# Kernel optimization log

Hardware: AMD Instinct MI355X
Metric: run time of the kernel (lower is better)

The kernel has to match this reference:

```python
import jax, jax.numpy as jnp
import numpy as np

# 3D PGA grade slices over the 16-component multivector (contiguous in standard basis order)
GRADE_SLICES = [(0, 1), (1, 5), (5, 11), (11, 15), (15, 16)]
GRADE_DIMS = [1, 4, 6, 4, 1]


def setup_inputs() -> dict:
    key = jax.random.key(0)
    ks = jax.random.split(key, 11)
    x = jax.random.normal(ks[0], (8, 2048, 128, 16), dtype=jnp.float32)
    inp = {"x": x}
    for g, d in enumerate(GRADE_DIMS):
        # match nn.Linear default init scale ~ U(-1/sqrt(d), 1/sqrt(d)); randn is fine for a numeric baseline
        inp[f"w{g}"] = jax.random.normal(ks[1 + 2 * g], (d, d), dtype=jnp.float32) / np.sqrt(d)
        inp[f"b{g}"] = jax.random.normal(ks[2 + 2 * g], (d,), dtype=jnp.float32) / np.sqrt(d)
    return inp


def reference(x, w0, b0, w1, b1, w2, b2, w3, b3, w4, b4):
    ws = [w0, w1, w2, w3, w4]
    bs = [b0, b1, b2, b3, b4]
    # Block-diagonal per-grade linear: gather slice, y = x_g @ W_g^T + b_g, scatter back.
    # Since grade index sets are contiguous, scatter == concatenate along last dim.
    outs = []
    for (lo, hi), w, b in zip(GRADE_SLICES, ws, bs):
        xg = x[..., lo:hi]                       # [..., d_g]
        outs.append(jnp.einsum("...i,oi->...o", xg, w) + b)
    return jnp.concatenate(outs, axis=-1)        # [..., 16]
```

## Files before the change

kernel.cpp:

```cpp
#include <hip/hip_runtime.h>


__global__ __launch_bounds__(256) void GradeWiseLinear_kernel(
    const float* __restrict__ x,
    const float* __restrict__ w0, const float* __restrict__ b0,
    const float* __restrict__ w1, const float* __restrict__ b1,
    const float* __restrict__ w2, const float* __restrict__ b2,
    const float* __restrict__ w3, const float* __restrict__ b3,
    const float* __restrict__ w4, const float* __restrict__ b4,
    float* __restrict__ out, int n4)
{
    __shared__ float s[86];
    {
        int t = threadIdx.x;
        if (t < 86) {
            float v;
            if      (t == 0)  v = w0[0];
            else if (t < 17)  v = w1[t - 1];
            else if (t < 53)  v = w2[t - 17];
            else if (t < 69)  v = w3[t - 53];
            else if (t == 69) v = w4[0];
            else if (t == 70) v = b0[0];
            else if (t < 75)  v = b1[t - 71];
            else if (t < 81)  v = b2[t - 75];
            else if (t < 85)  v = b3[t - 81];
            else              v = b4[0];
            s[t] = v;
        }
    }
    __syncthreads();

    int g = blockIdx.x * 256 + threadIdx.x;
    if (g >= n4) return;

    const int j = g & 3;
    const float4* x4 = (const float4*)x;

    float4 me = x4[g];
    float4 up = x4[g - (int)(j > 0)];
    float4 dn = x4[g + (int)(j < 3)];

    float o0, o1, o2, o3;

    if (j == 0) {
        o0 = s[70] + me.x * s[0];
        o1 = s[71] + me.y * s[1] + me.z * s[2]  + me.w * s[3]  + dn.x * s[4];
        o2 = s[72] + me.y * s[5] + me.z * s[6]  + me.w * s[7]  + dn.x * s[8];
        o3 = s[73] + me.y * s[9] + me.z * s[10] + me.w * s[11] + dn.x * s[12];
    } else if (j == 1) {
        o0 = s[74] + up.y * s[13] + up.z * s[14] + up.w * s[15] + me.x * s[16];
        o1 = s[75] + me.y * s[17] + me.z * s[18] + me.w * s[19]
                   + dn.x * s[20] + dn.y * s[21] + dn.z * s[22];
        o2 = s[76] + me.y * s[23] + me.z * s[24] + me.w * s[25]
                   + dn.x * s[26] + dn.y * s[27] + dn.z * s[28];
        o3 = s[77] + me.y * s[29] + me.z * s[30] + me.w * s[31]
                   + dn.x * s[32] + dn.y * s[33] + dn.z * s[34];
    } else if (j == 2) {
        o0 = s[78] + up.y * s[35] + up.z * s[36] + up.w * s[37]
                   + me.x * s[38] + me.y * s[39] + me.z * s[40];
        o1 = s[79] + up.y * s[41] + up.z * s[42] + up.w * s[43]
                   + me.x * s[44] + me.y * s[45] + me.z * s[46];
        o2 = s[80] + up.y * s[47] + up.z * s[48] + up.w * s[49]
                   + me.x * s[50] + me.y * s[51] + me.z * s[52];
        o3 = s[81] + me.w * s[53] + dn.x * s[54] + dn.y * s[55] + dn.z * s[56];
    } else {
        o0 = s[82] + up.w * s[57] + me.x * s[58] + me.y * s[59] + me.z * s[60];
        o1 = s[83] + up.w * s[61] + me.x * s[62] + me.y * s[63] + me.z * s[64];
        o2 = s[84] + up.w * s[65] + me.x * s[66] + me.y * s[67] + me.z * s[68];
        o3 = s[85] + me.w * s[69];
    }

    ((float4*)out)[g] = make_float4(o0, o1, o2, o3);
}

extern "C" void kernel_launch(void* const* d_in, const int* in_sizes, int n_in,
                              void* d_out, int out_size, void* d_ws, size_t ws_size,
                              hipStream_t stream) {
    const float* x  = (const float*)d_in[0];
    const float* w0 = (const float*)d_in[1];
    const float* b0 = (const float*)d_in[2];
    const float* w1 = (const float*)d_in[3];
    const float* b1 = (const float*)d_in[4];
    const float* w2 = (const float*)d_in[5];
    const float* b2 = (const float*)d_in[6];
    const float* w3 = (const float*)d_in[7];
    const float* b3 = (const float*)d_in[8];
    const float* w4 = (const float*)d_in[9];
    const float* b4 = (const float*)d_in[10];
    float* out = (float*)d_out;

    int n4 = in_sizes[0] / 4;
    int block = 256;
    int grid = (n4 + block - 1) / block;

    GradeWiseLinear_kernel<<<grid, block, 0, stream>>>(
        x, w0, b0, w1, b1, w2, b2, w3, b3, w4, b4, out, n4);
}
```

Baseline: 245.8 us.

## Process four float4s per thread, use wave shuffles for neighbors, nontemporal stores

Each thread now handles four float4 chunks strided by 256, and gets neighbor components through __shfl_up/__shfl_down instead of extra overlapping global loads. Outputs are written with nontemporal stores and the grid is a quarter of its former size. This removes the redundant up/dn loads and amortizes the per-block weight staging over more work. The bounds check is gone, so it relies on n4 being a multiple of 1024, and the shuffles rely on the 4-lane groups never straddling a wave boundary.

Result: no change. 248.1 us (+0.9%).

```diff
diff --git a/kernel.cpp b/kernel.cpp
--- a/kernel.cpp
+++ b/kernel.cpp
@@ -1,5 +1,7 @@
 #include <hip/hip_runtime.h>
 
+
+typedef float v4f __attribute__((ext_vector_type(4)));
 
 __global__ __launch_bounds__(256) void GradeWiseLinear_kernel(
     const float* __restrict__ x,
@@ -30,47 +32,73 @@
     }
     __syncthreads();
 
-    int g = blockIdx.x * 256 + threadIdx.x;
-    if (g >= n4) return;
+    const int t = threadIdx.x;
+    const int base = blockIdx.x * 1024 + t;
+    const int j = t & 3;
 
-    const int j = g & 3;
-    const float4* x4 = (const float4*)x;
+    const v4f* xv = (const v4f*)x;
 
-    float4 me = x4[g];
-    float4 up = x4[g - (int)(j > 0)];
-    float4 dn = x4[g + (int)(j < 3)];
+    v4f me[4];
+    #pragma unroll
+    for (int k = 0; k < 4; ++k) me[k] = xv[base + 256 * k];
 
-    float o0, o1, o2, o3;
+    float up_y[4], up_z[4], up_w[4], dn_x[4], dn_y[4], dn_z[4];
+    #pragma unroll
+    for (int k = 0; k < 4; ++k) {
+        up_y[k] = __shfl_up(me[k].y, 1);
+        up_z[k] = __shfl_up(me[k].z, 1);
+        up_w[k] = __shfl_up(me[k].w, 1);
+        dn_x[k] = __shfl_down(me[k].x, 1);
+        dn_y[k] = __shfl_down(me[k].y, 1);
+        dn_z[k] = __shfl_down(me[k].z, 1);
+    }
+
+    v4f r[4];
 
     if (j == 0) {
-        o0 = s[70] + me.x * s[0];
-        o1 = s[71] + me.y * s[1] + me.z * s[2]  + me.w * s[3]  + dn.x * s[4];
-        o2 = s[72] + me.y * s[5] + me.z * s[6]  + me.w * s[7]  + dn.x * s[8];
-        o3 = s[73] + me.y * s[9] + me.z * s[10] + me.w * s[11] + dn.x * s[12];
+        #pragma unroll
+        for (int k = 0; k < 4; ++k) {
+            r[k].x = s[70] + me[k].x * s[0];
+            r[k].y = s[71] + me[k].y * s[1] + me[k].z * s[2]  + me[k].w * s[3]  + dn_x[k] * s[4];
+            r[k].z = s[72] + me[k].y * s[5] + me[k].z * s[6]  + me[k].w * s[7]  + dn_x[k] * s[8];
+            r[k].w = s[73] + me[k].y * s[9] + me[k].z * s[10] + me[k].w * s[11] + dn_x[k] * s[12];
+        }
     } else if (j == 1) {
-        o0 = s[74] + up.y * s[13] + up.z * s[14] + up.w * s[15] + me.x * s[16];
-        o1 = s[75] + me.y * s[17] + me.z * s[18] + me.w * s[19]
-                   + dn.x * s[20] + dn.y * s[21] + dn.z * s[22];
-        o2 = s[76] + me.y * s[23] + me.z * s[24] + me.w * s[25]
-                   + dn.x * s[26] + dn.y * s[27] + dn.z * s[28];
-        o3 = s[77] + me.y * s[29] + me.z * s[30] + me.w * s[31]
-                   + dn.x * s[32] + dn.y * s[33] + dn.z * s[34];
+        #pragma unroll
+        for (int k = 0; k < 4; ++k) {
+            r[k].x = s[74] + up_y[k] * s[13] + up_z[k] * s[14] + up_w[k] * s[15] + me[k].x * s[16];
+            r[k].y = s[75] + me[k].y * s[17] + me[k].z * s[18] + me[k].w * s[19]
+                           + dn_x[k] * s[20] + dn_y[k] * s[21] + dn_z[k] * s[22];
+            r[k].z = s[76] + me[k].y * s[23] + me[k].z * s[24] + me[k].w * s[25]
+                           + dn_x[k] * s[26] + dn_y[k] * s[27] + dn_z[k] * s[28];
+            r[k].w = s[77] + me[k].y * s[29] + me[k].z * s[30] + me[k].w * s[31]
+                           + dn_x[k] * s[32] + dn_y[k] * s[33] + dn_z[k] * s[34];
+        }
     } else if (j == 2) {
-        o0 = s[78] + up.y * s[35] + up.z * s[36] + up.w * s[37]
-                   + me.x * s[38] + me.y * s[39] + me.z * s[40];
-        o1 = s[79] + up.y * s[41] + up.z * s[42] + up.w * s[43]
-                   + me.x * s[44] + me.y * s[45] + me.z * s[46];
-        o2 = s[80] + up.y * s[47] + up.z * s[48] + up.w * s[49]
-                   + me.x * s[50] + me.y * s[51] + me.z * s[52];
-        o3 = s[81] + me.w * s[53] + dn.x * s[54] + dn.y * s[55] + dn.z * s[56];
+        #pragma unroll
+        for (int k = 0; k < 4; ++k) {
+            r[k].x = s[78] + up_y[k] * s[35] + up_z[k] * s[36] + up_w[k] * s[37]
+                           + me[k].x * s[38] + me[k].y * s[39] + me[k].z * s[40];
+            r[k].y = s[79] + up_y[k] * s[41] + up_z[k] * s[42] + up_w[k] * s[43]
+                           + me[k].x * s[44] + me[k].y * s[45] + me[k].z * s[46];
+            r[k].z = s[80] + up_y[k] * s[47] + up_z[k] * s[48] + up_w[k] * s[49]
+                           + me[k].x * s[50] + me[k].y * s[51] + me[k].z * s[52];
+            r[k].w = s[81] + me[k].w * s[53] + dn_x[k] * s[54] + dn_y[k] * s[55] + dn_z[k] * s[56];
+        }
     } else {
-        o0 = s[82] + up.w * s[57] + me.x * s[58] + me.y * s[59] + me.z * s[60];
-        o1 = s[83] + up.w * s[61] + me.x * s[62] + me.y * s[63] + me.z * s[64];
-        o2 = s[84] + up.w * s[65] + me.x * s[66] + me.y * s[67] + me.z * s[68];
-        o3 = s[85] + me.w * s[69];
+        #pragma unroll
+        for (int k = 0; k < 4; ++k) {
+            r[k].x = s[82] + up_w[k] * s[57] + me[k].x * s[58] + me[k].y * s[59] + me[k].z * s[60];
+            r[k].y = s[83] + up_w[k] * s[61] + me[k].x * s[62] + me[k].y * s[63] + me[k].z * s[64];
+            r[k].z = s[84] + up_w[k] * s[65] + me[k].x * s[66] + me[k].y * s[67] + me[k].z * s[68];
+            r[k].w = s[85] + me[k].w * s[69];
+        }
     }
 
-    ((float4*)out)[g] = make_float4(o0, o1, o2, o3);
+    v4f* ov = (v4f*)out;
+    #pragma unroll
+    for (int k = 0; k < 4; ++k)
+        __builtin_nontemporal_store(r[k], ov + base + 256 * k);
 }
 
 extern "C" void kernel_launch(void* const* d_in, const int* in_sizes, int n_in,
@@ -91,7 +119,7 @@
 
     int n4 = in_sizes[0] / 4;
     int block = 256;
-    int grid = (n4 + block - 1) / block;
+    int grid = n4 / (block * 4);
 
     GradeWiseLinear_kernel<<<grid, block, 0, stream>>>(
         x, w0, b0, w1, b1, w2, b2, w3, b3, w4, b4, out, n4);
```
